# Performance work log

Hardware: AMD Instinct MI355X
Metric: run time of the kernel (lower is better)

The kernel has to match this reference:

```python
import jax, jax.numpy as jnp
import numpy as np

N = 524288          # total nodes
E = 1048576         # total directed edges (paired: fwd/bwd consecutive)
D = 128             # emb_dim
NUM_GRAPHS = 16384  # molecules in the batch


def mish(x):
    return x * jnp.tanh(jax.nn.softplus(x))


def segment_mean(x, seg, num_segments):
    s = jax.ops.segment_sum(x, seg, num_segments=num_segments)
    cnt = jax.ops.segment_sum(jnp.ones((x.shape[0],), x.dtype), seg, num_segments=num_segments)
    return s / jnp.maximum(cnt, 1.0)[:, None]


def setup_inputs() -> dict:
    key = jax.random.key(0)
    k = jax.random.split(key, 8)
    node_representation = jax.random.normal(k[0], (N, D), dtype=jnp.float32)
    batch = jnp.sort(jax.random.randint(k[1], (N,), 0, NUM_GRAPHS)).astype(jnp.int64)
    edge_index = jax.random.randint(k[2], (2, E), 0, N).astype(jnp.int64)
    s = 1.0 / np.sqrt(2 * D)
    W_node = jax.random.normal(k[3], (2 * D, D), dtype=jnp.float32) * s
    b_node = jnp.zeros((D,), jnp.float32)
    W_edge = jax.random.normal(k[4], (2 * D, D), dtype=jnp.float32) * s
    b_edge = jnp.zeros((D,), jnp.float32)
    W_pool = jax.random.normal(k[5], (D, D), dtype=jnp.float32) * (1.0 / np.sqrt(D))
    b_pool = jnp.zeros((D,), jnp.float32)
    return {"node_representation": node_representation, "batch": batch,
            "edge_index": edge_index, "W_node": W_node, "b_node": b_node,
            "W_edge": W_edge, "b_edge": b_edge, "W_pool": W_pool, "b_pool": b_pool}


def reference(node_representation, batch, edge_index, W_node, b_node,
              W_edge, b_edge, W_pool, b_pool):
    batch = batch.astype(jnp.int32)
    # global mean pool over graphs: [G, D]
    g = segment_mean(node_representation, batch, NUM_GRAPHS)
    # gather pooled graph vec back to nodes, concat, fuse
    node_cat = jnp.concatenate([node_representation, g[batch]], axis=1)  # [N, 2D]
    node_rep = mish(node_cat @ W_node + b_node)                          # [N, D]
    # edge fusion: gather endpoints, concat, fuse, then average paired edges
    e_cat = jnp.concatenate([node_rep[edge_index[0]], node_rep[edge_index[1]]], axis=1)  # [E, 2D]
    edge_rep = mish(e_cat @ W_edge + b_edge)                             # [E, D]
    edge_rep = edge_rep.reshape(-1, 2, D).mean(axis=1)                   # [E/2, D]
    # self edges: concat(node, node) through same edge fusion MLP
    self_edge_rep = mish(jnp.concatenate([node_rep, node_rep], axis=1) @ W_edge + b_edge)
    graph_rep = g @ W_pool + b_pool                                      # [G, D]
    return (node_rep, self_edge_rep, edge_rep, graph_rep)
```

## Files before the change

kernel.cpp:

```cpp
#include <hip/hip_runtime.h>
#include <stdint.h>


#define D128 128
#define NG 16384

typedef __attribute__((ext_vector_type(8))) short short8;
typedef __attribute__((ext_vector_type(4))) float f32x4;

__device__ __forceinline__ unsigned short f2bf(float f) {
  union { float f; unsigned int u; } v; v.f = f;
  unsigned int u = v.u;
  return (unsigned short)((u + 0x7fffu + ((u >> 16) & 1u)) >> 16);
}

__device__ __forceinline__ float mish_f(float v) {
  float u = __expf(fminf(v, 20.0f));
  float n = u * u + 2.0f * u;
  return v * n / (n + 2.0f);
}

__device__ __forceinline__ int swz(int r, int c) {
  return r * 128 + (((c ^ r) & 15) << 3);
}

__global__ void k_segmean(const float* __restrict__ x, const int* __restrict__ batch,
                          float* __restrict__ g, int N) {
  int gi = blockIdx.x;
  int lo = 0, hi = N;
  while (lo < hi) { int mid = (lo + hi) >> 1; if (batch[mid] < gi) lo = mid + 1; else hi = mid; }
  int start = lo;
  hi = N;
  while (lo < hi) { int mid = (lo + hi) >> 1; if (batch[mid] < gi + 1) lo = mid + 1; else hi = mid; }
  int end = lo;
  float s = 0.f;
  for (int r = start; r < end; ++r) s += x[(size_t)r * D128 + threadIdx.x];
  float cnt = (float)(end - start);
  g[(size_t)gi * D128 + threadIdx.x] = s / fmaxf(cnt, 1.0f);
}

__global__ void k_prep(const float* __restrict__ Wn, const float* __restrict__ We,
                       const float* __restrict__ Wp,
                       unsigned short* __restrict__ WnT, unsigned short* __restrict__ WnbT,
                       unsigned short* __restrict__ WpT, unsigned short* __restrict__ WsT,
                       unsigned short* __restrict__ WeT) {
  int id = blockIdx.x * 256 + threadIdx.x;
  if (id < 16384) {
    int n = id >> 7, k = id & 127;
    WnT[n * 128 + k] = f2bf(Wn[k * 128 + n]);
  } else if (id < 32768) {
    int t = id - 16384; int n = t >> 7, k = t & 127;
    WnbT[n * 128 + k] = f2bf(Wn[(k + 128) * 128 + n]);
  } else if (id < 49152) {
    int t = id - 32768; int n = t >> 7, k = t & 127;
    WpT[n * 128 + k] = f2bf(Wp[k * 128 + n]);
  } else if (id < 65536) {
    int t = id - 49152; int n = t >> 7, k = t & 127;
    WsT[n * 128 + k] = f2bf(We[k * 128 + n] + We[(k + 128) * 128 + n]);
  } else if (id < 98304) {
    int t = id - 65536; int n = t >> 8, k = t & 255;
    WeT[n * 256 + k] = f2bf(We[k * 128 + n]);
  }
}

__device__ __forceinline__ void stage_f32(unsigned short* lds, const float* src, int r0, int tid) {
#pragma unroll
  for (int it = 0; it < 8; ++it) {
    int id = it * 256 + tid;
    int r = id >> 4, c = id & 15;
    const float* p = src + (size_t)(r0 + r) * D128 + c * 8;
    float4 v0 = *(const float4*)p;
    float4 v1 = *(const float4*)(p + 4);
    short8 pk;
    pk[0] = (short)f2bf(v0.x); pk[1] = (short)f2bf(v0.y);
    pk[2] = (short)f2bf(v0.z); pk[3] = (short)f2bf(v0.w);
    pk[4] = (short)f2bf(v1.x); pk[5] = (short)f2bf(v1.y);
    pk[6] = (short)f2bf(v1.z); pk[7] = (short)f2bf(v1.w);
    *(short8*)&lds[swz(r, c)] = pk;
  }
}
__device__ __forceinline__ void stage_bf16(unsigned short* lds, const unsigned short* src,
                                           int stride, int k0, int tid) {
#pragma unroll
  for (int it = 0; it < 8; ++it) {
    int id = it * 256 + tid;
    int r = id >> 4, c = id & 15;
    *(short8*)&lds[swz(r, c)] = *(const short8*)(src + (size_t)r * stride + k0 + c * 8);
  }
}

#define MFMA_K128(A_lds, W_lds, acc, wr, wc, l15, quad)                                   \
  do {                                                                                    \
    _Pragma("unroll")                                                                     \
    for (int kc = 0; kc < 4; ++kc) {                                                      \
      short8 afr[4], bfr[4];                                                              \
      _Pragma("unroll")                                                                   \
      for (int i = 0; i < 4; ++i) afr[i] = *(const short8*)&A_lds[swz(wr + i*16 + l15, kc*4 + quad)]; \
      _Pragma("unroll")                                                                   \
      for (int j = 0; j < 4; ++j) bfr[j] = *(const short8*)&W_lds[swz(wc + j*16 + l15, kc*4 + quad)]; \
      _Pragma("unroll")                                                                   \
      for (int i = 0; i < 4; ++i)                                                         \
        _Pragma("unroll")                                                                 \
        for (int j = 0; j < 4; ++j)                                                       \
          acc[i][j] = __builtin_amdgcn_mfma_f32_16x16x32_bf16(afr[i], bfr[j], acc[i][j], 0, 0, 0); \
    }                                                                                     \
  } while (0)

template <bool WRITE_BF16>
__global__ __launch_bounds__(256, 2)
void k_node(const float* __restrict__ x, const int* __restrict__ batch,
            const float* __restrict__ h, const unsigned short* __restrict__ WnT,
            float* __restrict__ out0, unsigned short* __restrict__ nrb) {
  __shared__ unsigned short A_lds[16384];
  __shared__ unsigned short W_lds[16384];
  int tid = threadIdx.x;
  int m0 = blockIdx.x * 128;
  stage_f32(A_lds, x, m0, tid);
  stage_bf16(W_lds, WnT, 128, 0, tid);
  __syncthreads();
  int wave = tid >> 6, lane = tid & 63, l15 = lane & 15, quad = lane >> 4;
  int wr = (wave >> 1) * 64, wc = (wave & 1) * 64;
  f32x4 acc[4][4] = {};
  MFMA_K128(A_lds, W_lds, acc, wr, wc, l15, quad);
#pragma unroll
  for (int i = 0; i < 4; ++i) {
#pragma unroll
    for (int rr = 0; rr < 4; ++rr) {
      int grow = m0 + wr + i * 16 + quad * 4 + rr;
      int b = batch[grow];
      const float* hrow = h + (size_t)b * D128;
#pragma unroll
      for (int j = 0; j < 4; ++j) {
        int col = wc + j * 16 + l15;
        float m = mish_f(acc[i][j][rr] + hrow[col]);
        out0[(size_t)grow * D128 + col] = m;
        if (WRITE_BF16) nrb[(size_t)grow * D128 + col] = f2bf(m);
      }
    }
  }
}

template <bool SRCB, bool MISH>
__global__ __launch_bounds__(256, 2)
void k_rows(const void* __restrict__ src, const unsigned short* __restrict__ Wt,
            const float* __restrict__ bias, float* __restrict__ out) {
  __shared__ unsigned short A_lds[16384];
  __shared__ unsigned short W_lds[16384];
  int tid = threadIdx.x;
  int m0 = blockIdx.x * 128;
  if (SRCB) stage_bf16(A_lds, (const unsigned short*)src + (size_t)m0 * D128, 128, 0, tid);
  else      stage_f32(A_lds, (const float*)src, m0, tid);
  stage_bf16(W_lds, Wt, 128, 0, tid);
  __syncthreads();
  int wave = tid >> 6, lane = tid & 63, l15 = lane & 15, quad = lane >> 4;
  int wr = (wave >> 1) * 64, wc = (wave & 1) * 64;
  f32x4 acc[4][4] = {};
  MFMA_K128(A_lds, W_lds, acc, wr, wc, l15, quad);
#pragma unroll
  for (int i = 0; i < 4; ++i) {
#pragma unroll
    for (int rr = 0; rr < 4; ++rr) {
      int grow = m0 + wr + i * 16 + quad * 4 + rr;
#pragma unroll
      for (int j = 0; j < 4; ++j) {
        int col = wc + j * 16 + l15;
        float v = acc[i][j][rr] + bias[col];
        out[(size_t)grow * D128 + col] = MISH ? mish_f(v) : v;
      }
    }
  }
}

template <bool SRCB>
__global__ __launch_bounds__(256, 2)
void k_edge(const void* __restrict__ src, const int* __restrict__ eidx, int E,
            const unsigned short* __restrict__ WeT, const float* __restrict__ be,
            float* __restrict__ out2) {
  __shared__ unsigned short A_lds[16384];
  __shared__ unsigned short W_lds[16384];
  int tid = threadIdx.x;
  int e0 = blockIdx.x * 128;
  int wave = tid >> 6, lane = tid & 63, l15 = lane & 15, quad = lane >> 4;
  int wr = (wave >> 1) * 64, wc = (wave & 1) * 64;
  f32x4 acc[4][4] = {};
#pragma unroll
  for (int ph = 0; ph < 2; ++ph) {
    if (ph) __syncthreads();
#pragma unroll
    for (int it = 0; it < 8; ++it) {
      int id = it * 256 + tid;
      int r = id >> 4, c = id & 15;
      int row = eidx[ph * E + e0 + r];
      if (SRCB) {
        *(short8*)&A_lds[swz(r, c)] =
            *(const short8*)((const unsigned short*)src + (size_t)row * D128 + c * 8);
      } else {
        const float* p = (const float*)src + (size_t)row * D128 + c * 8;
        float4 v0 = *(const float4*)p;
        float4 v1 = *(const float4*)(p + 4);
        short8 pk;
        pk[0] = (short)f2bf(v0.x); pk[1] = (short)f2bf(v0.y);
        pk[2] = (short)f2bf(v0.z); pk[3] = (short)f2bf(v0.w);
        pk[4] = (short)f2bf(v1.x); pk[5] = (short)f2bf(v1.y);
        pk[6] = (short)f2bf(v1.z); pk[7] = (short)f2bf(v1.w);
        *(short8*)&A_lds[swz(r, c)] = pk;
      }
    }
    stage_bf16(W_lds, WeT, 256, ph * 128, tid);
    __syncthreads();
    MFMA_K128(A_lds, W_lds, acc, wr, wc, l15, quad);
  }
#pragma unroll
  for (int i = 0; i < 4; ++i) {
#pragma unroll
    for (int j = 0; j < 4; ++j) {
      int col = wc + j * 16 + l15;
      float bv = be[col];
      float m0v = mish_f(acc[i][j][0] + bv);
      float m1v = mish_f(acc[i][j][1] + bv);
      float m2v = mish_f(acc[i][j][2] + bv);
      float m3v = mish_f(acc[i][j][3] + bv);
      int rloc = wr + i * 16 + quad * 4;
      size_t p = (size_t)((e0 + rloc) >> 1);
      out2[p * D128 + col] = 0.5f * (m0v + m1v);
      out2[(p + 1) * D128 + col] = 0.5f * (m2v + m3v);
    }
  }
}

extern "C" void kernel_launch(void* const* d_in, const int* in_sizes, int n_in,
                              void* d_out, int out_size, void* d_ws, size_t ws_size,
                              hipStream_t stream) {
  const float* x  = (const float*)d_in[0];
  const int* batch = (const int*)d_in[1];
  const int* eidx  = (const int*)d_in[2];
  const float* Wn = (const float*)d_in[3];
  const float* bn = (const float*)d_in[4];
  const float* We = (const float*)d_in[5];
  const float* be = (const float*)d_in[6];
  const float* Wp = (const float*)d_in[7];
  const float* bp = (const float*)d_in[8];
  int N = in_sizes[0] / D128;
  int E = in_sizes[2] / 2;

  float* out  = (float*)d_out;
  float* out0 = out;
  float* out1 = out0 + (size_t)N * D128;
  float* out2 = out1 + (size_t)N * D128;
  float* out3 = out2 + (size_t)(E / 2) * D128;

  char* w = (char*)d_ws;
  float* g = (float*)w;                 w += (size_t)NG * D128 * 4;
  float* h = (float*)w;                 w += (size_t)NG * D128 * 4;
  unsigned short* WnT  = (unsigned short*)w; w += 16384 * 2;
  unsigned short* WnbT = (unsigned short*)w; w += 16384 * 2;
  unsigned short* WpT  = (unsigned short*)w; w += 16384 * 2;
  unsigned short* WsT  = (unsigned short*)w; w += 16384 * 2;
  unsigned short* WeT  = (unsigned short*)w; w += 32768 * 2;
  unsigned short* nrb  = (unsigned short*)w; w += (size_t)N * D128 * 2;
  bool cache = ws_size >= (size_t)(w - (char*)d_ws);

  k_segmean<<<NG, 128, 0, stream>>>(x, batch, g, N);
  k_prep<<<384, 256, 0, stream>>>(Wn, We, Wp, WnT, WnbT, WpT, WsT, WeT);
  k_rows<false, false><<<NG / 128, 256, 0, stream>>>(g, WnbT, bn, h);
  k_rows<false, false><<<NG / 128, 256, 0, stream>>>(g, WpT, bp, out3);
  if (cache) {
    k_node<true><<<N / 128, 256, 0, stream>>>(x, batch, h, WnT, out0, nrb);
    k_rows<true, true><<<N / 128, 256, 0, stream>>>(nrb, WsT, be, out1);
    k_edge<true><<<E / 128, 256, 0, stream>>>(nrb, eidx, E, WeT, be, out2);
  } else {
    k_node<false><<<N / 128, 256, 0, stream>>>(x, batch, h, WnT, out0, nullptr);
    k_rows<false, true><<<N / 128, 256, 0, stream>>>(out0, WsT, be, out1);
    k_edge<false><<<E / 128, 256, 0, stream>>>(out0, eidx, E, WeT, be, out2);
  }
}
```

Before: 1.317 ms.

## Fuse self-edge GEMM into node kernel, merge small GEMMs, prefetch edge gathers

The self-edge MLP now runs inside the node kernel: mish outputs are written as bf16 into shared memory and multiplied by the self-edge weights there, so the bf16 node rows no longer have to be read back by a separate kernel. The two small graph-level GEMMs are merged into one launch. In the bf16 edge path, the second endpoint's gather is loaded into registers while the first half's MFMAs run, overlapping global gather latency with compute at the cost of higher register pressure.

```diff
diff --git a/kernel.cpp b/kernel.cpp
--- a/kernel.cpp
+++ b/kernel.cpp
@@ -106,11 +106,48 @@
     }                                                                                     \
   } while (0)
 
+__global__ __launch_bounds__(256, 2)
+void k_small(const float* __restrict__ g,
+             const unsigned short* __restrict__ WnbT, const float* __restrict__ bn,
+             float* __restrict__ h,
+             const unsigned short* __restrict__ WpT, const float* __restrict__ bp,
+             float* __restrict__ out3) {
+  __shared__ unsigned short A_lds[16384];
+  __shared__ unsigned short W_lds[16384];
+  int tid = threadIdx.x;
+  bool second = blockIdx.x >= 128;
+  int m0 = (blockIdx.x & 127) * 128;
+  const unsigned short* Wt = second ? WpT : WnbT;
+  const float* bias = second ? bp : bn;
+  float* out = second ? out3 : h;
+  stage_f32(A_lds, g, m0, tid);
+  stage_bf16(W_lds, Wt, 128, 0, tid);
+  __syncthreads();
+  int wave = tid >> 6, lane = tid & 63, l15 = lane & 15, quad = lane >> 4;
+  int wr = (wave >> 1) * 64, wc = (wave & 1) * 64;
+  f32x4 acc[4][4] = {};
+  MFMA_K128(A_lds, W_lds, acc, wr, wc, l15, quad);
+#pragma unroll
+  for (int i = 0; i < 4; ++i) {
+#pragma unroll
+    for (int rr = 0; rr < 4; ++rr) {
+      int grow = m0 + wr + i * 16 + quad * 4 + rr;
+#pragma unroll
+      for (int j = 0; j < 4; ++j) {
+        int col = wc + j * 16 + l15;
+        out[(size_t)grow * D128 + col] = acc[i][j][rr] + bias[col];
+      }
+    }
+  }
+}
+
 template <bool WRITE_BF16>
 __global__ __launch_bounds__(256, 2)
 void k_node(const float* __restrict__ x, const int* __restrict__ batch,
             const float* __restrict__ h, const unsigned short* __restrict__ WnT,
-            float* __restrict__ out0, unsigned short* __restrict__ nrb) {
+            const unsigned short* __restrict__ WsT, const float* __restrict__ be,
+            float* __restrict__ out0, float* __restrict__ out1,
+            unsigned short* __restrict__ nrb) {
   __shared__ unsigned short A_lds[16384];
   __shared__ unsigned short W_lds[16384];
   int tid = threadIdx.x;
@@ -122,40 +159,30 @@
   int wr = (wave >> 1) * 64, wc = (wave & 1) * 64;
   f32x4 acc[4][4] = {};
   MFMA_K128(A_lds, W_lds, acc, wr, wc, l15, quad);
+  __syncthreads();
+  stage_bf16(W_lds, WsT, 128, 0, tid);
 #pragma unroll
   for (int i = 0; i < 4; ++i) {
 #pragma unroll
     for (int rr = 0; rr < 4; ++rr) {
-      int grow = m0 + wr + i * 16 + quad * 4 + rr;
+      int r = wr + i * 16 + quad * 4 + rr;
+      int grow = m0 + r;
       int b = batch[grow];
       const float* hrow = h + (size_t)b * D128;
 #pragma unroll
       for (int j = 0; j < 4; ++j) {
         int col = wc + j * 16 + l15;
         float m = mish_f(acc[i][j][rr] + hrow[col]);
+        unsigned short mb = f2bf(m);
         out0[(size_t)grow * D128 + col] = m;
-        if (WRITE_BF16) nrb[(size_t)grow * D128 + col] = f2bf(m);
+        if (WRITE_BF16) nrb[(size_t)grow * D128 + col] = mb;
+        A_lds[swz(r, col >> 3) + (col & 7)] = mb;
       }
     }
   }
-}
-
-template <bool SRCB, bool MISH>
-__global__ __launch_bounds__(256, 2)
-void k_rows(const void* __restrict__ src, const unsigned short* __restrict__ Wt,
-            const float* __restrict__ bias, float* __restrict__ out) {
-  __shared__ unsigned short A_lds[16384];
-  __shared__ unsigned short W_lds[16384];
-  int tid = threadIdx.x;
-  int m0 = blockIdx.x * 128;
-  if (SRCB) stage_bf16(A_lds, (const unsigned short*)src + (size_t)m0 * D128, 128, 0, tid);
-  else      stage_f32(A_lds, (const float*)src, m0, tid);
-  stage_bf16(W_lds, Wt, 128, 0, tid);
   __syncthreads();
-  int wave = tid >> 6, lane = tid & 63, l15 = lane & 15, quad = lane >> 4;
-  int wr = (wave >> 1) * 64, wc = (wave & 1) * 64;
-  f32x4 acc[4][4] = {};
-  MFMA_K128(A_lds, W_lds, acc, wr, wc, l15, quad);
+  f32x4 acc2[4][4] = {};
+  MFMA_K128(A_lds, W_lds, acc2, wr, wc, l15, quad);
 #pragma unroll
   for (int i = 0; i < 4; ++i) {
 #pragma unroll
@@ -164,8 +191,7 @@
 #pragma unroll
       for (int j = 0; j < 4; ++j) {
         int col = wc + j * 16 + l15;
-        float v = acc[i][j][rr] + bias[col];
-        out[(size_t)grow * D128 + col] = MISH ? mish_f(v) : v;
+        out1[(size_t)grow * D128 + col] = mish_f(acc2[i][j][rr] + be[col]);
       }
     }
   }
@@ -183,18 +209,45 @@
   int wave = tid >> 6, lane = tid & 63, l15 = lane & 15, quad = lane >> 4;
   int wr = (wave >> 1) * 64, wc = (wave & 1) * 64;
   f32x4 acc[4][4] = {};
-#pragma unroll
-  for (int ph = 0; ph < 2; ++ph) {
-    if (ph) __syncthreads();
+  if (SRCB) {
+    const unsigned short* s = (const unsigned short*)src;
 #pragma unroll
     for (int it = 0; it < 8; ++it) {
       int id = it * 256 + tid;
       int r = id >> 4, c = id & 15;
-      int row = eidx[ph * E + e0 + r];
-      if (SRCB) {
-        *(short8*)&A_lds[swz(r, c)] =
-            *(const short8*)((const unsigned short*)src + (size_t)row * D128 + c * 8);
-      } else {
+      int row = eidx[e0 + r];
+      *(short8*)&A_lds[swz(r, c)] = *(const short8*)(s + (size_t)row * D128 + c * 8);
+    }
+    stage_bf16(W_lds, WeT, 256, 0, tid);
+    __syncthreads();
+    short8 pre[8];
+#pragma unroll
+    for (int it = 0; it < 8; ++it) {
+      int id = it * 256 + tid;
+      int r = id >> 4, c = id & 15;
+      int row = eidx[E + e0 + r];
+      pre[it] = *(const short8*)(s + (size_t)row * D128 + c * 8);
+    }
+    MFMA_K128(A_lds, W_lds, acc, wr, wc, l15, quad);
+    __syncthreads();
+#pragma unroll
+    for (int it = 0; it < 8; ++it) {
+      int id = it * 256 + tid;
+      int r = id >> 4, c = id & 15;
+      *(short8*)&A_lds[swz(r, c)] = pre[it];
+    }
+    stage_bf16(W_lds, WeT, 256, 128, tid);
+    __syncthreads();
+    MFMA_K128(A_lds, W_lds, acc, wr, wc, l15, quad);
+  } else {
+#pragma unroll
+    for (int ph = 0; ph < 2; ++ph) {
+      if (ph) __syncthreads();
+#pragma unroll
+      for (int it = 0; it < 8; ++it) {
+        int id = it * 256 + tid;
+        int r = id >> 4, c = id & 15;
+        int row = eidx[ph * E + e0 + r];
         const float* p = (const float*)src + (size_t)row * D128 + c * 8;
         float4 v0 = *(const float4*)p;
         float4 v1 = *(const float4*)(p + 4);
@@ -205,10 +258,10 @@
         pk[6] = (short)f2bf(v1.z); pk[7] = (short)f2bf(v1.w);
         *(short8*)&A_lds[swz(r, c)] = pk;
       }
-    }
-    stage_bf16(W_lds, WeT, 256, ph * 128, tid);
-    __syncthreads();
-    MFMA_K128(A_lds, W_lds, acc, wr, wc, l15, quad);
+      stage_bf16(W_lds, WeT, 256, ph * 128, tid);
+      __syncthreads();
+      MFMA_K128(A_lds, W_lds, acc, wr, wc, l15, quad);
+    }
   }
 #pragma unroll
   for (int i = 0; i < 4; ++i) {
@@ -262,15 +315,12 @@
 
   k_segmean<<<NG, 128, 0, stream>>>(x, batch, g, N);
   k_prep<<<384, 256, 0, stream>>>(Wn, We, Wp, WnT, WnbT, WpT, WsT, WeT);
-  k_rows<false, false><<<NG / 128, 256, 0, stream>>>(g, WnbT, bn, h);
-  k_rows<false, false><<<NG / 128, 256, 0, stream>>>(g, WpT, bp, out3);
+  k_small<<<256, 256, 0, stream>>>(g, WnbT, bn, h, WpT, bp, out3);
   if (cache) {
-    k_node<true><<<N / 128, 256, 0, stream>>>(x, batch, h, WnT, out0, nrb);
-    k_rows<true, true><<<N / 128, 256, 0, stream>>>(nrb, WsT, be, out1);
+    k_node<true><<<N / 128, 256, 0, stream>>>(x, batch, h, WnT, WsT, be, out0, out1, nrb);
     k_edge<true><<<E / 128, 256, 0, stream>>>(nrb, eidx, E, WeT, be, out2);
   } else {
-    k_node<false><<<N / 128, 256, 0, stream>>>(x, batch, h, WnT, out0, nullptr);
-    k_rows<false, true><<<N / 128, 256, 0, stream>>>(out0, WsT, be, out1);
+    k_node<false><<<N / 128, 256, 0, stream>>>(x, batch, h, WnT, WsT, be, out0, out1, nullptr);
     k_edge<false><<<E / 128, 256, 0, stream>>>(out0, eidx, E, WeT, be, out2);
   }
 }
```

Measured after the change: 1.310 ms. No clear change (-0.5%).
